# Performance work log

Measured on AMD Instinct MI355X. Metric: run time of the kernel, lower is better.

Reference implementation:

```python
import jax, jax.numpy as jnp
import numpy as np
from jax import lax

NPOINT = 1024
K = 32
GN_GROUPS = 32
EPS = 1e-5


def farthest_point_sample(xyz, npoint):
    # xyz: (B,N,3) -> idx (B,npoint). Deterministic start at index 0.
    B, N, _ = xyz.shape
    dist0 = jnp.full((B, N), 1e10, dtype=xyz.dtype)
    far0 = jnp.zeros((B,), dtype=jnp.int32)
    barange = jnp.arange(B)

    def step(carry, _):
        dist, far = carry
        centroid = xyz[barange, far][:, None, :]              # (B,1,3)
        d = jnp.sum((xyz - centroid) ** 2, axis=-1)           # (B,N)
        dist = jnp.minimum(dist, d)
        far_new = jnp.argmax(dist, axis=-1).astype(jnp.int32)
        return (dist, far_new), far

    _, idxs = lax.scan(step, (dist0, far0), None, length=npoint)
    return idxs.T  # (B,npoint)


def conv1x1(x, w, b):
    # x: (B,Cin,M,K), w: (Cout,Cin)
    return jnp.einsum('oc,bcmk->bomk', w, x) + b[None, :, None, None]


def group_norm(x, gamma, beta, groups):
    B, C, M, Kk = x.shape
    xg = x.reshape(B, groups, C // groups, M, Kk)
    mu = xg.mean(axis=(2, 3, 4), keepdims=True)
    var = xg.var(axis=(2, 3, 4), keepdims=True)
    xg = (xg - mu) * lax.rsqrt(var + EPS)
    x = xg.reshape(B, C, M, Kk)
    return x * gamma[None, :, None, None] + beta[None, :, None, None]


def setup_inputs() -> dict:
    key = jax.random.key(0)
    ks = jax.random.split(key, 4)
    B, N, Cin = 16, 8192, 64
    hid, out_ch, in_total = 64, 128, 3 + Cin
    return {
        'xyz': jax.random.normal(ks[0], (B, N, 3), jnp.float32),
        'feat': jax.random.normal(ks[1], (B, N, Cin), jnp.float32),
        'w1': jax.random.normal(ks[2], (hid, in_total), jnp.float32) * 0.1,
        'b1': jnp.zeros((hid,), jnp.float32),
        'g1w': jnp.ones((hid,), jnp.float32),
        'g1b': jnp.zeros((hid,), jnp.float32),
        'w2': jax.random.normal(ks[3], (out_ch, hid), jnp.float32) * 0.1,
        'b2': jnp.zeros((out_ch,), jnp.float32),
        'g2w': jnp.ones((out_ch,), jnp.float32),
        'g2b': jnp.zeros((out_ch,), jnp.float32),
    }


def reference(xyz, feat, w1, b1, g1w, g1b, w2, b2, g2w, g2b):
    B, N, _ = xyz.shape
    M = min(NPOINT, N)
    k = min(K, N)

    fps_idx = farthest_point_sample(lax.stop_gradient(xyz), M)   # (B,M) ints
    batch = jnp.arange(B)[:, None]
    centroids = xyz[batch, fps_idx]                              # (B,M,3)

    # kNN via squared distances (same ordering as cdist p=2)
    d2 = (jnp.sum(centroids ** 2, -1)[:, :, None]
          + jnp.sum(xyz ** 2, -1)[:, None, :]
          - 2.0 * jnp.einsum('bmd,bnd->bmn', centroids, xyz))    # (B,M,N)
    knn_idx = lax.top_k(-d2, k)[1]                               # (B,M,k)

    b3 = jnp.arange(B)[:, None, None]
    group_xyz = xyz[b3, knn_idx]                                 # (B,M,k,3)
    delta = group_xyz - centroids[:, :, None, :]
    gfeat = feat[b3, knn_idx]                                    # (B,M,k,Cin)
    gf = jnp.concatenate([delta, gfeat], axis=-1)                # (B,M,k,3+Cin)
    x = jnp.transpose(gf, (0, 3, 1, 2))                          # (B,C,M,k)

    x = jax.nn.relu(group_norm(conv1x1(x, w1, b1), g1w, g1b, GN_GROUPS))
    x = jax.nn.relu(group_norm(conv1x1(x, w2, b2), g2w, g2b, GN_GROUPS))
    out = jnp.max(x, axis=-1)                                    # (B,out_ch,M)
    new_feat = jnp.transpose(out, (0, 2, 1))                     # (B,M,out_ch)
    return (centroids, new_feat)
```

## Files before the change

### kernel.cpp

```cpp
#include <hip/hip_runtime.h>
#include <cstdint>

#define BB 16
#define NN 8192
#define MM 1024
#define KNN 32
#define CIN 64
#define HID 64
#define OCH 128

#define KNN_OFF   0u
#define SUM1_OFF  524288u
#define SUM2_OFF  526336u
#define A1_OFF    530432u
#define D1_OFF    531456u
#define A2_OFF    532480u
#define D2_OFF    534528u
#define W2B_OFF   536576u
#define W1B_OFF   540672u
#define Y1_OFF    543744u
#define PTS4_OFF  Y1_OFF

typedef unsigned long long u64;
typedef float f32x4 __attribute__((ext_vector_type(4)));
typedef float f32x2 __attribute__((ext_vector_type(2)));
typedef short bf16x8 __attribute__((ext_vector_type(8)));

__device__ __forceinline__ unsigned short f2bf(float f) {
  union { float f; unsigned u; } v; v.f = f;
  unsigned r = v.u + 0x7FFFu + ((v.u >> 16) & 1u);
  return (unsigned short)(r >> 16);
}

__device__ __forceinline__ float bf2f(unsigned short u) {
  return __uint_as_float((unsigned)u << 16);
}

__global__ __launch_bounds__(256) void k0_init(const float* __restrict__ xyz,
                                               const float* __restrict__ w1,
                                               const float* __restrict__ w2,
                                               float* __restrict__ ws) {
  int t = blockIdx.x * 256 + threadIdx.x;
  if (t < 12288) ws[SUM1_OFF + t] = 0.0f;
  if (t < 4096) {
    unsigned lo = f2bf(w2[2 * t]);
    unsigned hi = f2bf(w2[2 * t + 1]);
    ((unsigned*)(ws + W2B_OFF))[t] = lo | (hi << 16);
  }
  if (t < 6144) {
    int n = t / 96, kk = t % 96;
    float val = 0.0f;
    if (kk < 3) val = w1[n * 67 + kk];
    else if (kk >= 4 && kk < 68) val = w1[n * 67 + kk - 1];
    ((unsigned short*)(ws + W1B_OFF))[t] = f2bf(val);
  }
  if (t < BB * NN) {
    #pragma clang fp contract(off)
    float x = xyz[(size_t)t * 3], y = xyz[(size_t)t * 3 + 1], z = xyz[(size_t)t * 3 + 2];
    ((float4*)(ws + PTS4_OFF))[t] = make_float4(x, y, z, (x * x + y * y) + z * z);
  }
}

__device__ __forceinline__ u64 wave_max_u64(u64 v) {
  #define DPP_RND(ctrl, rm)                                                     \
  {                                                                             \
    int lo_ = __builtin_amdgcn_update_dpp(0, (int)(unsigned)(v & 0xFFFFFFFFull),\
                                          ctrl, rm, 0xf, true);                 \
    int hi_ = __builtin_amdgcn_update_dpp(0, (int)(unsigned)(v >> 32),          \
                                          ctrl, rm, 0xf, true);                 \
    u64 o_ = ((u64)(unsigned)hi_ << 32) | (unsigned)lo_;                        \
    v = o_ > v ? o_ : v;                                                        \
  }
  DPP_RND(0x111, 0xf)
  DPP_RND(0x112, 0xf)
  DPP_RND(0x114, 0xf)
  DPP_RND(0x118, 0xf)
  DPP_RND(0x142, 0xa)
  DPP_RND(0x143, 0xc)
  #undef DPP_RND
  return v;
}

__global__ __launch_bounds__(256) void fps_kernel(const float* __restrict__ xyz,
                                                  float* __restrict__ cent) {
  #pragma clang fp contract(off)
  __shared__ float4 sp4[NN];
  __shared__ u64 slots[MM];
  const int b = blockIdx.x, tid = threadIdx.x;
  const float* xp = xyz + (size_t)b * NN * 3;
  f32x2 px[16], py[16], pz[16];
  float dist0[16], dist1[16];
  #pragma unroll
  for (int i = 0; i < 16; ++i) {
    int n0 = tid + (2 * i) * 256, n1 = tid + (2 * i + 1) * 256;
    float x0 = xp[n0 * 3], y0 = xp[n0 * 3 + 1], z0 = xp[n0 * 3 + 2];
    float x1 = xp[n1 * 3], y1 = xp[n1 * 3 + 1], z1 = xp[n1 * 3 + 2];
    px[i] = (f32x2){x0, x1}; py[i] = (f32x2){y0, y1}; pz[i] = (f32x2){z0, z1};
    sp4[n0] = make_float4(x0, y0, z0, 0.0f);
    sp4[n1] = make_float4(x1, y1, z1, 0.0f);
    dist0[i] = 1e10f; dist1[i] = 1e10f;
  }
  for (int s = tid; s < MM; s += 256) slots[s] = 0ull;
  __syncthreads();
  int far = 0;
  for (int step = 0; step < MM; ++step) {
    float4 c4 = sp4[far];
    f32x2 cx = (f32x2){c4.x, c4.x}, cy = (f32x2){c4.y, c4.y}, cz = (f32x2){c4.z, c4.z};
    float best = -1.0f; int bi = 0;
    #pragma unroll
    for (int i = 0; i < 16; ++i) {
      f32x2 dx = px[i] - cx, dy = py[i] - cy, dz = pz[i] - cz;
      f32x2 d = (dx * dx + dy * dy) + dz * dz;
      float dm0 = fminf(dist0[i], d.x);
      float dm1 = fminf(dist1[i], d.y);
      dist0[i] = dm0; dist1[i] = dm1;
      if (dm0 > best) { best = dm0; bi = tid + (2 * i) * 256; }
      if (dm1 > best) { best = dm1; bi = tid + (2 * i + 1) * 256; }
    }
    u64 key = ((u64)__float_as_uint(best) << 32) | (unsigned)(8191 - bi);
    key = wave_max_u64(key);
    if ((tid & 63) == 63) atomicMax(&slots[step], key);
    __syncthreads();
    far = 8191 - (int)(unsigned)(slots[step] & 0xFFFFFFFFull);
  }
  float* co = cent + (size_t)b * MM * 3;
  for (int s = tid; s < MM; s += 256) {
    int fs = (s == 0) ? 0 : (8191 - (int)(unsigned)(slots[s - 1] & 0xFFFFFFFFull));
    float4 c = sp4[fs];
    co[s * 3 + 0] = c.x; co[s * 3 + 1] = c.y; co[s * 3 + 2] = c.z;
  }
}

__global__ __launch_bounds__(512) void knn_kernel(const float4* __restrict__ pts4,
                                                  const float* __restrict__ cent,
                                                  int* __restrict__ knnout) {
  #pragma clang fp contract(off)
  __shared__ __align__(16) char smem[65536];
  unsigned* blo = (unsigned*)smem;
  unsigned* bhi = (unsigned*)(smem + 32768);
  u64* marea = (u64*)smem;
  const int tid = threadIdx.x;
  const int lane = tid & 63;
  const int w = tid >> 6;
  const int b = blockIdx.x >> 4;
  const int m = ((blockIdx.x & 15) << 6) + lane;
  const float* cp = cent + ((size_t)b * MM + m) * 3;
  float cx = cp[0], cy = cp[1], cz = cp[2];
  float cn2 = (cx * cx + cy * cy) + cz * cz;
  u64 key[32];
  {
    u64 initk = ((u64)(__float_as_uint(3e38f) ^ 0x80000000u) << 32) | 0xFFFFFFFFull;
    #pragma unroll
    for (int j = 0; j < 32; ++j) key[j] = initk;
  }
  float kthf = 3e38f;

  auto insert = [&](u64 cand) {
    bool cprev = false; u64 kprev = 0;
    #pragma unroll
    for (int j = 0; j < 32; ++j) {
      bool cj = cand < key[j];
      u64 cur = key[j];
      u64 nv = cj ? cand : cur;
      key[j] = cprev ? kprev : nv;
      cprev = cj; kprev = cur;
    }
    unsigned hb = (unsigned)(key[31] >> 32);
    unsigned ob = (hb & 0x80000000u) ? (hb ^ 0x80000000u) : ~hb;
    kthf = __uint_as_float(ob);
  };

  int cnt = 0;
  auto flush = [&]() {
    int mc = cnt;
    #pragma unroll
    for (int off = 1; off < 64; off <<= 1) { int o = __shfl_xor(mc, off); mc = o > mc ? o : mc; }
    for (int i = 0; i < mc; ++i) {
      u64 cand = ((u64)bhi[i * 512 + tid] << 32) | blo[i * 512 + tid];
      if (i < cnt && cand < key[31]) insert(cand);
    }
    cnt = 0;
  };

  const int nbase = __builtin_amdgcn_readfirstlane(w * 1024);
  const float4* pb = pts4 + (size_t)b * NN + nbase;
  for (int n0 = 0; n0 < 1024; n0 += 8) {
    #pragma unroll
    for (int j = 0; j < 8; ++j) {
      int n = n0 + j;
      float4 p = pb[n];
      float dot = fmaf(cz, p.z, fmaf(cy, p.y, cx * p.x));
      float d2 = (cn2 + p.w) - 2.0f * dot;
      if (d2 <= kthf) {
        unsigned db = __float_as_uint(d2);
        unsigned fk = db ^ (((int)db < 0) ? 0xFFFFFFFFu : 0x80000000u);
        blo[cnt * 512 + tid] = (unsigned)(nbase + n);
        bhi[cnt * 512 + tid] = fk;
        cnt++;
      }
    }
    if (__ballot(cnt >= 9)) flush();
  }
  flush();
  __syncthreads();

  auto publish = [&](int a) {
    u64* ap = marea + a * 2048;
    #pragma unroll
    for (int j = 0; j < 32; ++j) ap[j * 64 + lane] = key[j];
  };
  auto merge_from = [&](int a) {
    u64* ap = marea + a * 2048;
    for (int j = 0; j < 32; ++j) {
      u64 cand = ap[j * 64 + lane];
      if (cand < key[31]) insert(cand);
    }
  };
  if (w & 1) publish(w >> 1);
  __syncthreads();
  if (!(w & 1)) merge_from(w >> 1);
  __syncthreads();
  if (w == 2) publish(0);
  if (w == 6) publish(1);
  __syncthreads();
  if (w == 0) merge_from(0);
  if (w == 4) merge_from(1);
  __syncthreads();
  if (w == 4) publish(0);
  __syncthreads();
  if (w == 0) {
    merge_from(0);
    int* op = knnout + ((size_t)b * MM + m) * KNN;
    #pragma unroll
    for (int j = 0; j < 32; ++j) op[j] = (int)(key[j] & 0xFFFFFFFFull);
  }
}

__global__ __launch_bounds__(256) void conv1_kernel(const float* __restrict__ xyz,
                                                    const float* __restrict__ feat,
                                                    const float* __restrict__ cent,
                                                    const int* __restrict__ knn,
                                                    const unsigned short* __restrict__ w1b,
                                                    const float* __restrict__ b1,
                                                    float* __restrict__ y1,
                                                    float* __restrict__ sums1) {
  __shared__ __align__(16) unsigned short gsm[4][32 * 104];
  __shared__ float s1acc[64], q1acc[64];
  const int tid = threadIdx.x, lane = tid & 63, w = tid >> 6;
  const int wid = blockIdx.x * 4 + w;
  const int b = wid >> 10;
  unsigned short* gf = gsm[w];

  if (tid < 64) { s1acc[tid] = 0.0f; q1acc[tid] = 0.0f; }
  __syncthreads();

  int idxv = 0;
  if (lane < 32) idxv = knn[(size_t)wid * 32 + lane];

  {
    int row = lane >> 1, h = (lane & 1) * 16;
    ushort4 z4 = {0, 0, 0, 0};
    *(ushort4*)(gf + row * 104 + 64 + h + 0)  = z4;
    *(ushort4*)(gf + row * 104 + 64 + h + 4)  = z4;
    *(ushort4*)(gf + row * 104 + 64 + h + 8)  = z4;
    *(ushort4*)(gf + row * 104 + 64 + h + 12) = z4;
  }
  const float* cp = cent + (size_t)wid * 3;
  float ccx = cp[0], ccy = cp[1], ccz = cp[2];
  if (lane < 32) {
    const float* pp = xyz + ((size_t)b * NN + idxv) * 3;
    ushort4 dv;
    dv.x = f2bf(pp[0] - ccx); dv.y = f2bf(pp[1] - ccy); dv.z = f2bf(pp[2] - ccz);
    dv.w = 0;
    *(ushort4*)(gf + lane * 104) = dv;
  }
  const float4* fb = (const float4*)feat;
  #pragma unroll
  for (int i = 0; i < 8; ++i) {
    int v = i * 64 + lane;
    int row = v >> 4, part = v & 15;
    int ridx = __shfl(idxv, row);
    float4 f4 = fb[(size_t)(b * NN + ridx) * 16 + part];
    ushort4 s;
    s.x = f2bf(f4.x); s.y = f2bf(f4.y); s.z = f2bf(f4.z); s.w = f2bf(f4.w);
    *(ushort4*)(gf + row * 104 + 4 + part * 4) = s;
  }
  __builtin_amdgcn_s_waitcnt(0);
  __builtin_amdgcn_wave_barrier();

  const int quad = lane >> 4, lr = lane & 15;
  bf16x8 bw[4][3];
  float b1v[4];
  #pragma unroll
  for (int nt = 0; nt < 4; ++nt) {
    #pragma unroll
    for (int ks = 0; ks < 3; ++ks)
      bw[nt][ks] = *(const bf16x8*)(w1b + (size_t)(nt * 16 + lr) * 96 + ks * 32 + quad * 8);
    b1v[nt] = b1[nt * 16 + lr];
  }
  f32x4 acc[2][4];
  #pragma unroll
  for (int mt = 0; mt < 2; ++mt)
    #pragma unroll
    for (int nt = 0; nt < 4; ++nt)
      acc[mt][nt] = (f32x4){0.f, 0.f, 0.f, 0.f};
  #pragma unroll
  for (int ks = 0; ks < 3; ++ks) {
    bf16x8 a0 = *(const bf16x8*)(gf + (0 + lr) * 104 + ks * 32 + quad * 8);
    bf16x8 a1 = *(const bf16x8*)(gf + (16 + lr) * 104 + ks * 32 + quad * 8);
    #pragma unroll
    for (int nt = 0; nt < 4; ++nt) {
      acc[0][nt] = __builtin_amdgcn_mfma_f32_16x16x32_bf16(a0, bw[nt][ks], acc[0][nt], 0, 0, 0);
      acc[1][nt] = __builtin_amdgcn_mfma_f32_16x16x32_bf16(a1, bw[nt][ks], acc[1][nt], 0, 0, 0);
    }
  }
  unsigned short* yo16 = (unsigned short*)(y1 + (size_t)wid * 1024);
  float s_nt[4] = {0.f, 0.f, 0.f, 0.f};
  float q_nt[4] = {0.f, 0.f, 0.f, 0.f};
  #pragma unroll
  for (int mt = 0; mt < 2; ++mt)
    #pragma unroll
    for (int rg = 0; rg < 4; ++rg) {
      int row = mt * 16 + quad * 4 + rg;
      #pragma unroll
      for (int nt = 0; nt < 4; ++nt) {
        float z = acc[mt][nt][rg] + b1v[nt];
        yo16[row * 64 + nt * 16 + lr] = f2bf(z);
        s_nt[nt] += z;
        q_nt[nt] = fmaf(z, z, q_nt[nt]);
      }
    }
  #pragma unroll
  for (int nt = 0; nt < 4; ++nt) {
    float s = s_nt[nt], q = q_nt[nt];
    s += __shfl_xor(s, 16); s += __shfl_xor(s, 32);
    q += __shfl_xor(q, 16); q += __shfl_xor(q, 32);
    if (quad == 0) {
      atomicAdd(&s1acc[nt * 16 + lr], s);
      atomicAdd(&q1acc[nt * 16 + lr], q);
    }
  }
  __syncthreads();
  if (tid < 64) {
    atomicAdd(&sums1[b * 128 + tid], s1acc[tid]);
    atomicAdd(&sums1[b * 128 + 64 + tid], q1acc[tid]);
  }
}

__global__ void coeffs_kernel(const float* __restrict__ sums,
                              const float* __restrict__ gamma,
                              const float* __restrict__ beta,
                              float* __restrict__ a, float* __restrict__ d,
                              int nch, int cpg, float invn) {
  int t = blockIdx.x * blockDim.x + threadIdx.x;
  if (t >= BB * nch) return;
  int b = t / nch, c = t % nch, g = c / cpg;
  float S = 0, Q = 0;
  for (int j = 0; j < cpg; ++j) {
    S += sums[b * 2 * nch + g * cpg + j];
    Q += sums[b * 2 * nch + nch + g * cpg + j];
  }
  float mu = S * invn;
  float var = Q * invn - mu * mu;
  float rs = 1.0f / sqrtf(var + 1e-5f);
  float ga = gamma[c];
  a[t] = rs * ga;
  d[t] = beta[c] - mu * rs * ga;
}

struct Conv2Frag {
  bf16x8 bfr[8][2];
  float  b2v[8];
};

__device__ __forceinline__ void load_w2_frags(const unsigned short* __restrict__ w2b,
                                              const float* __restrict__ b2,
                                              int lane, Conv2Frag& F) {
  const int quad = lane >> 4, lr = lane & 15;
  #pragma unroll
  for (int nt = 0; nt < 8; ++nt) {
    #pragma unroll
    for (int t = 0; t < 2; ++t)
      F.bfr[nt][t] = *(const bf16x8*)(w2b + (size_t)(nt * 16 + lr) * 64 + t * 32 + quad * 8);
    F.b2v[nt] = b2[nt * 16 + lr];
  }
}

__device__ __forceinline__ void conv2_wave_mfma(const float* __restrict__ y1,
                                                const float* __restrict__ a1,
                                                const float* __restrict__ d1,
                                                unsigned short* __restrict__ hrow,
                                                int wid, int b, int lane,
                                                const Conv2Frag& F,
                                                f32x4 acc[2][8]) {
  const int quad = lane >> 4, lr = lane & 15;
  const int r = lane >> 1, c0 = (lane & 1) * 32;
  const unsigned short* yrow16 =
      (const unsigned short*)(y1 + (size_t)wid * 1024) + r * 64 + c0;
  const float4* ap = (const float4*)(a1 + b * 64 + c0);
  const float4* dp = (const float4*)(d1 + b * 64 + c0);
  #pragma unroll
  for (int gg = 0; gg < 4; ++gg) {
    bf16x8 yv = *(const bf16x8*)(yrow16 + gg * 8);
    float4 av0 = ap[gg * 2],     dv0 = dp[gg * 2];
    float4 av1 = ap[gg * 2 + 1], dv1 = dp[gg * 2 + 1];
    ushort4 s0, s1;
    s0.x = f2bf(fmaxf(0.0f, fmaf(bf2f((unsigned short)yv[0]), av0.x, dv0.x)));
    s0.y = f2bf(fmaxf(0.0f, fmaf(bf2f((unsigned short)yv[1]), av0.y, dv0.y)));
    s0.z = f2bf(fmaxf(0.0f, fmaf(bf2f((unsigned short)yv[2]), av0.z, dv0.z)));
    s0.w = f2bf(fmaxf(0.0f, fmaf(bf2f((unsigned short)yv[3]), av0.w, dv0.w)));
    s1.x = f2bf(fmaxf(0.0f, fmaf(bf2f((unsigned short)yv[4]), av1.x, dv1.x)));
    s1.y = f2bf(fmaxf(0.0f, fmaf(bf2f((unsigned short)yv[5]), av1.y, dv1.y)));
    s1.z = f2bf(fmaxf(0.0f, fmaf(bf2f((unsigned short)yv[6]), av1.z, dv1.z)));
    s1.w = f2bf(fmaxf(0.0f, fmaf(bf2f((unsigned short)yv[7]), av1.w, dv1.w)));
    *(ushort4*)(hrow + r * 72 + c0 + 8 * gg)     = s0;
    *(ushort4*)(hrow + r * 72 + c0 + 8 * gg + 4) = s1;
  }
  __builtin_amdgcn_s_waitcnt(0);
  __builtin_amdgcn_wave_barrier();
  #pragma unroll
  for (int mt = 0; mt < 2; ++mt)
    #pragma unroll
    for (int nt = 0; nt < 8; ++nt)
      acc[mt][nt] = (f32x4){0.f, 0.f, 0.f, 0.f};
  #pragma unroll
  for (int t = 0; t < 2; ++t) {
    bf16x8 a0 = *(const bf16x8*)(hrow + (0 + lr) * 72 + t * 32 + quad * 8);
    bf16x8 a1f = *(const bf16x8*)(hrow + (16 + lr) * 72 + t * 32 + quad * 8);
    #pragma unroll
    for (int nt = 0; nt < 8; ++nt) {
      acc[0][nt] = __builtin_amdgcn_mfma_f32_16x16x32_bf16(a0,  F.bfr[nt][t], acc[0][nt], 0, 0, 0);
      acc[1][nt] = __builtin_amdgcn_mfma_f32_16x16x32_bf16(a1f, F.bfr[nt][t], acc[1][nt], 0, 0, 0);
    }
  }
}

__global__ __launch_bounds__(256) void conv2_stats_kernel(float* __restrict__ y1,
                                                          const float* __restrict__ a1,
                                                          const float* __restrict__ d1,
                                                          const unsigned short* __restrict__ w2b,
                                                          const float* __restrict__ b2,
                                                          float* __restrict__ sums2) {
  __shared__ __align__(16) unsigned short hsm[4][32 * 72];
  __shared__ float sacc[128], qacc[128];
  const int tid = threadIdx.x, lane = tid & 63, w = tid >> 6;
  const int wid = blockIdx.x * 4 + w;
  const int b = blockIdx.x >> 8;
  if (tid < 128) { sacc[tid] = 0.0f; qacc[tid] = 0.0f; }
  __syncthreads();
  Conv2Frag F;
  load_w2_frags(w2b, b2, lane, F);
  f32x4 acc[2][8];
  conv2_wave_mfma(y1, a1, d1, hsm[w], wid, b, lane, F, acc);
  const int lr = lane & 15;
  float zmx[8], zmn[8];
  #pragma unroll
  for (int nt = 0; nt < 8; ++nt) {
    float s = 0, q = 0, mx = -3e38f, mn = 3e38f;
    #pragma unroll
    for (int mt = 0; mt < 2; ++mt)
      #pragma unroll
      for (int rg = 0; rg < 4; ++rg) {
        float z = acc[mt][nt][rg] + F.b2v[nt];
        s += z; q = fmaf(z, z, q);
        mx = fmaxf(mx, z); mn = fminf(mn, z);
      }
    atomicAdd(&sacc[nt * 16 + lr], s);
    atomicAdd(&qacc[nt * 16 + lr], q);
    mx = fmaxf(mx, __shfl_xor(mx, 16)); mx = fmaxf(mx, __shfl_xor(mx, 32));
    mn = fminf(mn, __shfl_xor(mn, 16)); mn = fminf(mn, __shfl_xor(mn, 32));
    zmx[nt] = mx; zmn[nt] = mn;
  }
  if (lane < 16) {
    float* zp = y1 + (size_t)wid * 1024;
    #pragma unroll
    for (int nt = 0; nt < 8; ++nt) {
      zp[nt * 16 + lr] = zmx[nt];
      zp[128 + nt * 16 + lr] = zmn[nt];
    }
  }
  __syncthreads();
  if (tid < 128) {
    atomicAdd(&sums2[b * 256 + tid], sacc[tid]);
    atomicAdd(&sums2[b * 256 + 128 + tid], qacc[tid]);
  }
}

__global__ __launch_bounds__(256) void final_lite(const float* __restrict__ y1,
                                                  const float* __restrict__ a2,
                                                  const float* __restrict__ d2,
                                                  float* __restrict__ nf) {
  int idx = blockIdx.x * 256 + threadIdx.x;
  int wid = idx >> 7, c = idx & 127;
  int b = wid >> 10;
  const float* zp = y1 + (size_t)wid * 1024;
  float zmx = zp[c];
  float zmn = zp[128 + c];
  float az = a2[b * 128 + c], dz = d2[b * 128 + c];
  float z = (az >= 0.0f) ? zmx : zmn;
  nf[(size_t)wid * 128 + c] = fmaxf(0.0f, fmaf(z, az, dz));
}

extern "C" void kernel_launch(void* const* d_in, const int* in_sizes, int n_in,
                              void* d_out, int out_size, void* d_ws, size_t ws_size,
                              hipStream_t stream) {
  const float* xyz  = (const float*)d_in[0];
  const float* feat = (const float*)d_in[1];
  const float* w1   = (const float*)d_in[2];
  const float* b1   = (const float*)d_in[3];
  const float* g1w  = (const float*)d_in[4];
  const float* g1b  = (const float*)d_in[5];
  const float* w2   = (const float*)d_in[6];
  const float* b2   = (const float*)d_in[7];
  const float* g2w  = (const float*)d_in[8];
  const float* g2b  = (const float*)d_in[9];
  float* ws = (float*)d_ws;
  float* cent = (float*)d_out;
  float* nf   = (float*)d_out + BB * MM * 3;
  const float4* pts4 = (const float4*)(ws + PTS4_OFF);
  int*   knn   = (int*)(ws + KNN_OFF);
  float* sums1 = ws + SUM1_OFF;
  float* sums2 = ws + SUM2_OFF;
  float* a1 = ws + A1_OFF; float* d1 = ws + D1_OFF;
  float* a2 = ws + A2_OFF; float* d2 = ws + D2_OFF;
  const unsigned short* w2b = (const unsigned short*)(ws + W2B_OFF);
  const unsigned short* w1b = (const unsigned short*)(ws + W1B_OFF);
  float* y1 = ws + Y1_OFF;

  hipLaunchKernelGGL(k0_init, dim3(512), dim3(256), 0, stream, xyz, w1, w2, ws);
  hipLaunchKernelGGL(fps_kernel, dim3(16), dim3(256), 0, stream, xyz, cent);
  hipLaunchKernelGGL(knn_kernel, dim3(256), dim3(512), 0, stream, pts4, cent, knn);
  hipLaunchKernelGGL(conv1_kernel, dim3(4096), dim3(256), 0, stream,
                     xyz, feat, cent, knn, w1b, b1, y1, sums1);
  hipLaunchKernelGGL(coeffs_kernel, dim3(4), dim3(256), 0, stream,
                     sums1, g1w, g1b, a1, d1, 64, 2, 1.0f / 65536.0f);
  hipLaunchKernelGGL(conv2_stats_kernel, dim3(4096), dim3(256), 0, stream,
                     y1, a1, d1, w2b, b2, sums2);
  hipLaunchKernelGGL(coeffs_kernel, dim3(8), dim3(256), 0, stream,
                     sums2, g2w, g2b, a2, d2, 128, 4, 1.0f / 131072.0f);
  hipLaunchKernelGGL(final_lite, dim3(8192), dim3(256), 0, stream,
                     y1, a2, d2, nf);
}
```

Measured before the change: 1.489 ms.

## Prepack features to bf16, fuse GroupNorm coeffs, and streamline FPS argmax reduction

k0_init now converts the feature tensor to packed bf16 in workspace, so the conv1 gather reads half as many bytes and skips per-element conversion. The two coeffs_kernel launches are removed; each conv2 and final block recomputes its GroupNorm scale and shift in shared memory. In FPS, the per-element index tracking becomes a max followed by a separate min-index search, and the cross-wave atomicMax on slots is replaced by double-buffered per-wave shared-memory slots that every thread reads, dropping the slot clearing. The trade-offs are a full extra pass over the features inside the timed init kernel, redundant coefficient math in every block, and extra compare and select work in the FPS inner loop.

New measurement: 1.592 ms. +6.9%, slower.

```diff
diff --git a/kernel.cpp b/kernel.cpp
--- a/kernel.cpp
+++ b/kernel.cpp
@@ -20,6 +20,7 @@
 #define W1B_OFF   540672u
 #define Y1_OFF    543744u
 #define PTS4_OFF  Y1_OFF
+#define FEAT16_OFF (Y1_OFF + 16777216u)
 
 typedef unsigned long long u64;
 typedef float f32x4 __attribute__((ext_vector_type(4)));
@@ -37,6 +38,7 @@
 }
 
 __global__ __launch_bounds__(256) void k0_init(const float* __restrict__ xyz,
+                                               const float* __restrict__ feat,
                                                const float* __restrict__ w1,
                                                const float* __restrict__ w2,
                                                float* __restrict__ ws) {
@@ -59,6 +61,11 @@
     float x = xyz[(size_t)t * 3], y = xyz[(size_t)t * 3 + 1], z = xyz[(size_t)t * 3 + 2];
     ((float4*)(ws + PTS4_OFF))[t] = make_float4(x, y, z, (x * x + y * y) + z * z);
   }
+  if (t < 4194304) {
+    float2 fv = *(const float2*)(feat + 2 * (size_t)t);
+    unsigned lo = f2bf(fv.x), hi = f2bf(fv.y);
+    ((unsigned*)(ws + FEAT16_OFF))[t] = lo | (hi << 16);
+  }
 }
 
 __device__ __forceinline__ u64 wave_max_u64(u64 v) {
@@ -86,7 +93,9 @@
   #pragma clang fp contract(off)
   __shared__ float4 sp4[NN];
   __shared__ u64 slots[MM];
+  __shared__ u64 wred[2][4];
   const int b = blockIdx.x, tid = threadIdx.x;
+  const int w = tid >> 6;
   const float* xp = xyz + (size_t)b * NN * 3;
   f32x2 px[16], py[16], pz[16];
   float dist0[16], dist1[16];
@@ -100,13 +109,12 @@
     sp4[n1] = make_float4(x1, y1, z1, 0.0f);
     dist0[i] = 1e10f; dist1[i] = 1e10f;
   }
-  for (int s = tid; s < MM; s += 256) slots[s] = 0ull;
   __syncthreads();
   int far = 0;
   for (int step = 0; step < MM; ++step) {
     float4 c4 = sp4[far];
     f32x2 cx = (f32x2){c4.x, c4.x}, cy = (f32x2){c4.y, c4.y}, cz = (f32x2){c4.z, c4.z};
-    float best = -1.0f; int bi = 0;
+    float best = -1.0f;
     #pragma unroll
     for (int i = 0; i < 16; ++i) {
       f32x2 dx = px[i] - cx, dy = py[i] - cy, dz = pz[i] - cz;
@@ -114,15 +122,34 @@
       float dm0 = fminf(dist0[i], d.x);
       float dm1 = fminf(dist1[i], d.y);
       dist0[i] = dm0; dist1[i] = dm1;
-      if (dm0 > best) { best = dm0; bi = tid + (2 * i) * 256; }
-      if (dm1 > best) { best = dm1; bi = tid + (2 * i + 1) * 256; }
-    }
+      best = fmaxf(fmaxf(best, dm0), dm1);
+    }
+    unsigned sel[16];
+    #pragma unroll
+    for (int i = 0; i < 16; ++i) {
+      unsigned s0 = (dist0[i] == best) ? (unsigned)(2 * i) : 63u;
+      unsigned s1 = (dist1[i] == best) ? (unsigned)(2 * i + 1) : 63u;
+      sel[i] = s0 < s1 ? s0 : s1;
+    }
+    #pragma unroll
+    for (int st = 8; st >= 1; st >>= 1)
+      #pragma unroll
+      for (int i = 0; i < st; ++i)
+        sel[i] = sel[i] < sel[i + st] ? sel[i] : sel[i + st];
+    int bi = tid + (int)(sel[0] << 8);
     u64 key = ((u64)__float_as_uint(best) << 32) | (unsigned)(8191 - bi);
     key = wave_max_u64(key);
-    if ((tid & 63) == 63) atomicMax(&slots[step], key);
+    const int p = step & 1;
+    if ((tid & 63) == 63) wred[p][w] = key;
     __syncthreads();
-    far = 8191 - (int)(unsigned)(slots[step] & 0xFFFFFFFFull);
-  }
+    u64 k0 = wred[p][0], k1 = wred[p][1], k2 = wred[p][2], k3 = wred[p][3];
+    u64 m01 = k0 > k1 ? k0 : k1;
+    u64 m23 = k2 > k3 ? k2 : k3;
+    u64 bk = m01 > m23 ? m01 : m23;
+    if (tid == 0) slots[step] = bk;
+    far = 8191 - (int)(unsigned)(bk & 0xFFFFFFFFull);
+  }
+  __syncthreads();
   float* co = cent + (size_t)b * MM * 3;
   for (int s = tid; s < MM; s += 256) {
     int fs = (s == 0) ? 0 : (8191 - (int)(unsigned)(slots[s - 1] & 0xFFFFFFFFull));
@@ -237,7 +264,7 @@
 }
 
 __global__ __launch_bounds__(256) void conv1_kernel(const float* __restrict__ xyz,
-                                                    const float* __restrict__ feat,
+                                                    const unsigned short* __restrict__ feat16,
                                                     const float* __restrict__ cent,
                                                     const int* __restrict__ knn,
                                                     const unsigned short* __restrict__ w1b,
@@ -274,16 +301,15 @@
     dv.w = 0;
     *(ushort4*)(gf + lane * 104) = dv;
   }
-  const float4* fb = (const float4*)feat;
-  #pragma unroll
-  for (int i = 0; i < 8; ++i) {
+  const unsigned short* fb = feat16 + (size_t)b * NN * 64;
+  #pragma unroll
+  for (int i = 0; i < 4; ++i) {
     int v = i * 64 + lane;
-    int row = v >> 4, part = v & 15;
+    int row = v >> 3, part = v & 7;
     int ridx = __shfl(idxv, row);
-    float4 f4 = fb[(size_t)(b * NN + ridx) * 16 + part];
-    ushort4 s;
-    s.x = f2bf(f4.x); s.y = f2bf(f4.y); s.z = f2bf(f4.z); s.w = f2bf(f4.w);
-    *(ushort4*)(gf + row * 104 + 4 + part * 4) = s;
+    uint4 fv = *(const uint4*)(fb + (size_t)ridx * 64 + part * 8);
+    *(uint2*)(gf + row * 104 + 4 + part * 8)     = make_uint2(fv.x, fv.y);
+    *(uint2*)(gf + row * 104 + 4 + part * 8 + 4) = make_uint2(fv.z, fv.w);
   }
   __builtin_amdgcn_s_waitcnt(0);
   __builtin_amdgcn_wave_barrier();
@@ -347,27 +373,6 @@
   }
 }
 
-__global__ void coeffs_kernel(const float* __restrict__ sums,
-                              const float* __restrict__ gamma,
-                              const float* __restrict__ beta,
-                              float* __restrict__ a, float* __restrict__ d,
-                              int nch, int cpg, float invn) {
-  int t = blockIdx.x * blockDim.x + threadIdx.x;
-  if (t >= BB * nch) return;
-  int b = t / nch, c = t % nch, g = c / cpg;
-  float S = 0, Q = 0;
-  for (int j = 0; j < cpg; ++j) {
-    S += sums[b * 2 * nch + g * cpg + j];
-    Q += sums[b * 2 * nch + nch + g * cpg + j];
-  }
-  float mu = S * invn;
-  float var = Q * invn - mu * mu;
-  float rs = 1.0f / sqrtf(var + 1e-5f);
-  float ga = gamma[c];
-  a[t] = rs * ga;
-  d[t] = beta[c] - mu * rs * ga;
-}
-
 struct Conv2Frag {
   bf16x8 bfr[8][2];
   float  b2v[8];
@@ -387,18 +392,18 @@
 }
 
 __device__ __forceinline__ void conv2_wave_mfma(const float* __restrict__ y1,
-                                                const float* __restrict__ a1,
-                                                const float* __restrict__ d1,
+                                                const float* a1s,
+                                                const float* d1s,
                                                 unsigned short* __restrict__ hrow,
-                                                int wid, int b, int lane,
+                                                int wid, int lane,
                                                 const Conv2Frag& F,
                                                 f32x4 acc[2][8]) {
   const int quad = lane >> 4, lr = lane & 15;
   const int r = lane >> 1, c0 = (lane & 1) * 32;
   const unsigned short* yrow16 =
       (const unsigned short*)(y1 + (size_t)wid * 1024) + r * 64 + c0;
-  const float4* ap = (const float4*)(a1 + b * 64 + c0);
-  const float4* dp = (const float4*)(d1 + b * 64 + c0);
+  const float4* ap = (const float4*)(a1s + c0);
+  const float4* dp = (const float4*)(d1s + c0);
   #pragma unroll
   for (int gg = 0; gg < 4; ++gg) {
     bf16x8 yv = *(const bf16x8*)(yrow16 + gg * 8);
@@ -436,22 +441,35 @@
 }
 
 __global__ __launch_bounds__(256) void conv2_stats_kernel(float* __restrict__ y1,
-                                                          const float* __restrict__ a1,
-                                                          const float* __restrict__ d1,
+                                                          const float* __restrict__ sums1,
+                                                          const float* __restrict__ g1w,
+                                                          const float* __restrict__ g1b,
                                                           const unsigned short* __restrict__ w2b,
                                                           const float* __restrict__ b2,
                                                           float* __restrict__ sums2) {
   __shared__ __align__(16) unsigned short hsm[4][32 * 72];
   __shared__ float sacc[128], qacc[128];
+  __shared__ float a1s[64], d1s[64];
   const int tid = threadIdx.x, lane = tid & 63, w = tid >> 6;
   const int wid = blockIdx.x * 4 + w;
   const int b = blockIdx.x >> 8;
   if (tid < 128) { sacc[tid] = 0.0f; qacc[tid] = 0.0f; }
+  if (tid < 64) {
+    int c = tid, g = c >> 1;
+    float S = sums1[b * 128 + g * 2] + sums1[b * 128 + g * 2 + 1];
+    float Q = sums1[b * 128 + 64 + g * 2] + sums1[b * 128 + 64 + g * 2 + 1];
+    float mu = S * (1.0f / 65536.0f);
+    float var = Q * (1.0f / 65536.0f) - mu * mu;
+    float rs = 1.0f / sqrtf(var + 1e-5f);
+    float ga = g1w[c];
+    a1s[c] = rs * ga;
+    d1s[c] = g1b[c] - mu * rs * ga;
+  }
   __syncthreads();
   Conv2Frag F;
   load_w2_frags(w2b, b2, lane, F);
   f32x4 acc[2][8];
-  conv2_wave_mfma(y1, a1, d1, hsm[w], wid, b, lane, F, acc);
+  conv2_wave_mfma(y1, a1s, d1s, hsm[w], wid, lane, F, acc);
   const int lr = lane & 15;
   float zmx[8], zmn[8];
   #pragma unroll
@@ -487,16 +505,33 @@
 }
 
 __global__ __launch_bounds__(256) void final_lite(const float* __restrict__ y1,
-                                                  const float* __restrict__ a2,
-                                                  const float* __restrict__ d2,
+                                                  const float* __restrict__ sums2,
+                                                  const float* __restrict__ g2w,
+                                                  const float* __restrict__ g2b,
                                                   float* __restrict__ nf) {
-  int idx = blockIdx.x * 256 + threadIdx.x;
-  int wid = idx >> 7, c = idx & 127;
-  int b = wid >> 10;
+  __shared__ float a2s[128], d2s[128];
+  const int tid = threadIdx.x;
+  const int wid0 = blockIdx.x * 2;
+  const int b = wid0 >> 10;
+  if (tid < 128) {
+    int c = tid, g = c >> 2;
+    float S = ((sums2[b * 256 + g * 4] + sums2[b * 256 + g * 4 + 1])
+               + sums2[b * 256 + g * 4 + 2]) + sums2[b * 256 + g * 4 + 3];
+    float Q = ((sums2[b * 256 + 128 + g * 4] + sums2[b * 256 + 128 + g * 4 + 1])
+               + sums2[b * 256 + 128 + g * 4 + 2]) + sums2[b * 256 + 128 + g * 4 + 3];
+    float mu = S * (1.0f / 131072.0f);
+    float var = Q * (1.0f / 131072.0f) - mu * mu;
+    float rs = 1.0f / sqrtf(var + 1e-5f);
+    float ga = g2w[c];
+    a2s[c] = rs * ga;
+    d2s[c] = g2b[c] - mu * rs * ga;
+  }
+  __syncthreads();
+  int wid = wid0 + (tid >> 7), c = tid & 127;
   const float* zp = y1 + (size_t)wid * 1024;
   float zmx = zp[c];
   float zmn = zp[128 + c];
-  float az = a2[b * 128 + c], dz = d2[b * 128 + c];
+  float az = a2s[c], dz = d2s[c];
   float z = (az >= 0.0f) ? zmx : zmn;
   nf[(size_t)wid * 128 + c] = fmaxf(0.0f, fmaf(z, az, dz));
 }
@@ -521,23 +556,18 @@
   int*   knn   = (int*)(ws + KNN_OFF);
   float* sums1 = ws + SUM1_OFF;
   float* sums2 = ws + SUM2_OFF;
-  float* a1 = ws + A1_OFF; float* d1 = ws + D1_OFF;
-  float* a2 = ws + A2_OFF; float* d2 = ws + D2_OFF;
   const unsigned short* w2b = (const unsigned short*)(ws + W2B_OFF);
   const unsigned short* w1b = (const unsigned short*)(ws + W1B_OFF);
+  const unsigned short* feat16 = (const unsigned short*)(ws + FEAT16_OFF);
   float* y1 = ws + Y1_OFF;
 
-  hipLaunchKernelGGL(k0_init, dim3(512), dim3(256), 0, stream, xyz, w1, w2, ws);
+  hipLaunchKernelGGL(k0_init, dim3(16384), dim3(256), 0, stream, xyz, feat, w1, w2, ws);
   hipLaunchKernelGGL(fps_kernel, dim3(16), dim3(256), 0, stream, xyz, cent);
   hipLaunchKernelGGL(knn_kernel, dim3(256), dim3(512), 0, stream, pts4, cent, knn);
   hipLaunchKernelGGL(conv1_kernel, dim3(4096), dim3(256), 0, stream,
-                     xyz, feat, cent, knn, w1b, b1, y1, sums1);
-  hipLaunchKernelGGL(coeffs_kernel, dim3(4), dim3(256), 0, stream,
-                     sums1, g1w, g1b, a1, d1, 64, 2, 1.0f / 65536.0f);
+                     xyz, feat16, cent, knn, w1b, b1, y1, sums1);
   hipLaunchKernelGGL(conv2_stats_kernel, dim3(4096), dim3(256), 0, stream,
-                     y1, a1, d1, w2b, b2, sums2);
-  hipLaunchKernelGGL(coeffs_kernel, dim3(8), dim3(256), 0, stream,
-                     sums2, g2w, g2b, a2, d2, 128, 4, 1.0f / 131072.0f);
+                     y1, sums1, g1w, g1b, w2b, b2, sums2);
   hipLaunchKernelGGL(final_lite, dim3(8192), dim3(256), 0, stream,
-                     y1, a2, d2, nf);
-}
+                     y1, sums2, g2w, g2b, nf);
+}
```
